# Performance work log

Hardware: AMD Instinct MI355X
Metric: run time of the kernel (lower is better)

## Reference

```python
import jax, jax.numpy as jnp
import numpy as np

KH = KW = 3
STRIDE, PAD, DIL = 1, 1, 1
HEADS, DG, CLIP, C = 12, 12, 2, 192
B, H, W = 4, 48, 48


def _linear_chw(x, w, b):
    # x: (n, d, c, h, w); Linear over channel dim (module rearranges to channels-last)
    return jnp.einsum('ndchw,oc->ndohw', x, w) + b[None, None, :, None, None]


def _deform_attn(q, kv, offset):
    # q: (b,1,C,H,W); kv: (b,clip,2C,H,W); offset: (b,clip,DG*K*2,H,W)
    b = q.shape[0]
    K = KH * KW
    HW = H * W
    dim = C // HEADS
    cg = 2 * C // DG  # channels per deformable group in kv (standard im2col split)
    ky = jnp.repeat(jnp.arange(KH), KW).astype(jnp.float32)  # (K,)
    kx = jnp.tile(jnp.arange(KW), KH).astype(jnp.float32)
    off = offset.reshape(b, CLIP, DG, K, 2, H, W)  # per-group [y,x] pairs per tap
    base_y = jnp.arange(H, dtype=jnp.float32)[None, :, None] * STRIDE - PAD + ky[:, None, None] * DIL  # (K,H,1)
    base_x = jnp.arange(W, dtype=jnp.float32)[None, None, :] * STRIDE - PAD + kx[:, None, None] * DIL  # (K,1,W)
    py = base_y + off[:, :, :, :, 0]  # (b,clip,dg,K,H,W)
    px = base_x + off[:, :, :, :, 1]
    kv_g = kv.reshape(b, CLIP, DG, cg, HW)

    y0 = jnp.floor(py)
    x0 = jnp.floor(px)
    wy1 = py - y0
    wx1 = px - x0

    def corner(yi, xi, wgt):
        valid = (yi >= 0) & (yi <= H - 1) & (xi >= 0) & (xi <= W - 1)
        idx = (jnp.clip(yi, 0, H - 1) * W + jnp.clip(xi, 0, W - 1)).astype(jnp.int32)
        idx = jnp.broadcast_to(idx.reshape(b, CLIP, DG, K, 1, HW), (b, CLIP, DG, K, cg, HW))
        src = jnp.broadcast_to(kv_g[:, :, :, None], (b, CLIP, DG, K, cg, HW))
        vals = jnp.take_along_axis(src, idx, axis=-1)  # gather over source pixels
        w_eff = (wgt * valid.astype(wgt.dtype)).reshape(b, CLIP, DG, K, 1, HW)
        return vals * w_eff

    s = (corner(y0, x0, (1 - wy1) * (1 - wx1))
         + corner(y0, x0 + 1, (1 - wy1) * wx1)
         + corner(y0 + 1, x0, wy1 * (1 - wx1))
         + corner(y0 + 1, x0 + 1, wy1 * wx1))  # (b,clip,dg,K,cg,HW)
    # restore channel order: (dg, cg) -> 2C = [C of k, C of v]
    s = s.transpose(0, 1, 2, 4, 3, 5).reshape(b, CLIP, 2, HEADS, dim, K, HW)
    ks, vs = s[:, :, 0], s[:, :, 1]  # (b,clip,heads,dim,K,HW)
    qh = q.reshape(b, HEADS, dim, HW) * (dim ** -0.5)
    scores = jnp.einsum('bhdn,bchdkn->bnhck', qh, ks)  # (b,HW,heads,clip,K)
    attn = jax.nn.softmax(scores.reshape(b, HW, HEADS, CLIP * K), axis=-1).reshape(b, HW, HEADS, CLIP, K)
    out = jnp.einsum('bnhck,bchdkn->bhdn', attn, vs)
    return out.reshape(b, 1, C, H, W)


def setup_inputs() -> dict:
    key = jax.random.key(0)
    ks = jax.random.split(key, 16)
    sd = 0.02
    return {
        'q': jax.random.normal(ks[0], (B, 1, C, H, W), jnp.float32),
        'k': jax.random.normal(ks[1], (B, CLIP, C, H, W), jnp.float32),
        'v': jax.random.normal(ks[2], (B, CLIP, C, H, W), jnp.float32),
        'offset': jax.random.normal(ks[3], (B, CLIP, DG * KH * KW * 2, H, W), jnp.float32),
        'wq': jax.random.normal(ks[4], (C, C), jnp.float32) * sd,
        'bq': jnp.zeros((C,), jnp.float32),
        'wk': jax.random.normal(ks[5], (C, C), jnp.float32) * sd,
        'bk': jnp.zeros((C,), jnp.float32),
        'wv': jax.random.normal(ks[6], (C, C), jnp.float32) * sd,
        'bv': jnp.zeros((C,), jnp.float32),
        'w1': jax.random.normal(ks[7], (2 * C, C), jnp.float32) * sd,
        'b1': jnp.zeros((2 * C,), jnp.float32),
        'w2': jax.random.normal(ks[8], (C, 2 * C), jnp.float32) * sd,
        'b2': jnp.zeros((C,), jnp.float32),
    }


def reference(q, k, v, offset, wq, bq, wk, bk, wv, bv, w1, b1, w2, b2):
    qp = _linear_chw(q, wq, bq)
    kv = jnp.concatenate([_linear_chw(k, wk, bk), _linear_chw(v, wv, bv)], axis=2)
    o = _deform_attn(qp, kv, offset)
    h = jnp.einsum('ndchw,oc->ndohw', o, w1) + b1[None, None, :, None, None]
    h = jax.nn.gelu(h, approximate=False)
    m = jnp.einsum('ndchw,oc->ndohw', h, w2) + b2[None, None, :, None, None]
    return o + m
```

## Files before the change

kernel.cpp:

```cpp
#include <hip/hip_runtime.h>

#define HW 2304
#define WID 48

typedef __attribute__((ext_vector_type(8))) short bf16x8;
typedef __attribute__((ext_vector_type(4))) float f32x4;
typedef __attribute__((ext_vector_type(2))) _Float16 half2v;

__device__ __forceinline__ half2v pk_h2(float lo, float hi) {
  return __builtin_bit_cast(half2v, __builtin_amdgcn_cvt_pkrtz(lo, hi));
}

__device__ __forceinline__ unsigned pack_bf2(float lo, float hi) {
  unsigned a = __builtin_bit_cast(unsigned, lo);
  unsigned b = __builtin_bit_cast(unsigned, hi);
  a = (a + 0x7FFFu + ((a >> 16) & 1u)) >> 16;
  b = (b + 0x7FFFu + ((b >> 16) & 1u)) >> 16;
  return a | (b << 16);
}
__device__ __forceinline__ unsigned short bf16_of(float x) {
  unsigned u = __builtin_bit_cast(unsigned, x);
  u = (u + 0x7FFFu + ((u >> 16) & 1u)) >> 16;
  return (unsigned short)u;
}
__device__ __forceinline__ unsigned short f16_of(float x) {
  _Float16 h = (_Float16)x;
  return __builtin_bit_cast(unsigned short, h);
}
__device__ __forceinline__ float lo_bf(unsigned u) {
  return __builtin_bit_cast(float, u << 16);
}
__device__ __forceinline__ float hi_bf(unsigned u) {
  return __builtin_bit_cast(float, u & 0xFFFF0000u);
}

__global__ __launch_bounds__(256) void prep_w(
    const float* __restrict__ wq, const float* __restrict__ wk,
    const float* __restrict__ wv, const float* __restrict__ w1,
    const float* __restrict__ w2, unsigned* __restrict__ wf)
{
  int fid = blockIdx.x * 4 + (threadIdx.x >> 6);
  int l = threadIdx.x & 63;
  const float* src; int K; int base;
  if (fid < 72)       { src = wq; K = 192; base = 0; }
  else if (fid < 144) { src = wk; K = 192; base = 72; }
  else if (fid < 216) { src = wv; K = 192; base = 144; }
  else if (fid < 360) { src = w1; K = 192; base = 216; }
  else                { src = w2; K = 384; base = 360; }
  int local = fid - base;
  int KS = K / 32;
  int nf = local / KS, ks = local % KS;
  int row = nf * 16 + (l & 15);
  int c0 = ks * 32 + (l >> 4) * 8;
  const float* p = src + (size_t)row * K + c0;
  float4 v0 = *(const float4*)p;
  float4 v1 = *(const float4*)(p + 4);
  unsigned* dst = wf + ((size_t)fid * 64 + l) * 4;
  dst[0] = pack_bf2(v0.x, v0.y);
  dst[1] = pack_bf2(v0.z, v0.w);
  dst[2] = pack_bf2(v1.x, v1.y);
  dst[3] = pack_bf2(v1.z, v1.w);
}

__global__ __launch_bounds__(256) void proj_mfma(
    const float* __restrict__ q, const float* __restrict__ k, const float* __restrict__ v,
    const unsigned* __restrict__ wf,
    const float* __restrict__ bq, const float* __restrict__ bk, const float* __restrict__ bv,
    float* __restrict__ qp, unsigned short* __restrict__ kvh)
{
  __shared__ unsigned lds[64 * 100];
  int slab = blockIdx.y;
  const float* in; const unsigned* wfr; const float* bias;
  float* outf = nullptr; unsigned short* outh = nullptr;
  int mode;
  if (slab < 4) {
    in = q + (size_t)slab * 192 * HW; wfr = wf; bias = bq;
    outf = qp + (size_t)slab * HW * 192; mode = 0;
  } else if (slab < 12) {
    int c = slab - 4;
    in = k + (size_t)c * 192 * HW; wfr = wf + 72 * 256; bias = bk;
    outh = kvh + (size_t)c * HW * 384; mode = 1;
  } else {
    int c = slab - 12;
    in = v + (size_t)c * 192 * HW; wfr = wf + 144 * 256; bias = bv;
    outh = kvh + (size_t)c * HW * 384 + 192; mode = 2;
  }
  const int n0 = blockIdx.x * 64;
  const int t = threadIdx.x;
  const int w = t >> 6, l = t & 63;

  {
    int pix = t & 63;
    int cp0 = t >> 6;
    const float* s0 = in + n0 + pix;
#pragma unroll
    for (int i = 0; i < 24; ++i) {
      int cp = cp0 * 24 + i;
      float lo = s0[(size_t)(2 * cp) * HW];
      float hi = s0[(size_t)(2 * cp + 1) * HW];
      lds[pix * 100 + cp] = pack_bf2(lo, hi);
    }
  }

  bf16x8 wfrag[6][3];
#pragma unroll
  for (int ks = 0; ks < 6; ++ks)
#pragma unroll
    for (int nfi = 0; nfi < 3; ++nfi) {
      int nf = w * 3 + nfi;
      wfrag[ks][nfi] = ((const bf16x8*)wfr)[(nf * 6 + ks) * 64 + l];
    }

  __syncthreads();

  f32x4 acc[3][4];
#pragma unroll
  for (int a = 0; a < 3; ++a)
#pragma unroll
    for (int m = 0; m < 4; ++m) acc[a][m] = (f32x4){0.f, 0.f, 0.f, 0.f};

#pragma unroll
  for (int ks = 0; ks < 6; ++ks) {
    bf16x8 af[4];
#pragma unroll
    for (int mf = 0; mf < 4; ++mf)
      af[mf] = *(const bf16x8*)&lds[(mf * 16 + (l & 15)) * 100 + ks * 16 + (l >> 4) * 4];
#pragma unroll
    for (int nfi = 0; nfi < 3; ++nfi)
#pragma unroll
      for (int mf = 0; mf < 4; ++mf)
        acc[nfi][mf] = __builtin_amdgcn_mfma_f32_16x16x32_bf16(af[mf], wfrag[ks][nfi], acc[nfi][mf], 0, 0, 0);
  }

#pragma unroll
  for (int nfi = 0; nfi < 3; ++nfi) {
    int oc = (w * 3 + nfi) * 16 + (l & 15);
    float bs = bias[oc];
    if (mode == 0) {
#pragma unroll
      for (int mf = 0; mf < 4; ++mf) {
        int pixb = n0 + mf * 16 + (l >> 4) * 4;
#pragma unroll
        for (int j = 0; j < 4; ++j)
          outf[(size_t)(pixb + j) * 192 + oc] = acc[nfi][mf][j] + bs;
      }
    } else if (mode == 1) {
#pragma unroll
      for (int mf = 0; mf < 4; ++mf) {
        int pixb = n0 + mf * 16 + (l >> 4) * 4;
#pragma unroll
        for (int j = 0; j < 4; ++j)
          outh[(size_t)(pixb + j) * 384 + oc] = f16_of(acc[nfi][mf][j] + bs);
      }
    } else {
#pragma unroll
      for (int mf = 0; mf < 4; ++mf) {
        int pixb = n0 + mf * 16 + (l >> 4) * 4;
#pragma unroll
        for (int j = 0; j < 4; ++j)
          outh[(size_t)(pixb + j) * 384 + oc] = bf16_of(acc[nfi][mf][j] + bs);
      }
    }
  }
}

__global__ __launch_bounds__(256, 4) void attn_kernel(
    const float* __restrict__ qp, const unsigned short* __restrict__ kvh,
    const float* __restrict__ offs, float* __restrict__ o_ws)
{
  __shared__ uint4 rec[2][2][9][32];
  const int t = threadIdx.x;
  const int g = blockIdx.x & 7;
  const int pos = blockIdx.x >> 3;
  const int b = g >> 1;
  const int half = g & 1;
  const int pk = pos / 36;
  const int tile = pos % 36;
  const int n_base = half * 1152 + tile * 32;

#pragma unroll
  for (int i = 0; i < 5; ++i) {
    int rid = t + i * 256;
    if (rid < 1152) {
      int rpix = rid & 31;
      int rest = rid >> 5;
      int rtap = rest % 9;
      int rq = rest / 9;
      int rclip = rq & 1;
      int dgsel = rq >> 1;
      int rn = n_base + rpix;
      int rh = rn / WID, rw = rn % WID;
      int dg = pk + dgsel * 6;
      const float* ob = offs + ((size_t)(b * 2 + rclip) * 216 + (size_t)(dg * 9 + rtap) * 2) * HW + rn;
      float oy = ob[0];
      float ox = ob[HW];
      float py = (float)(rh - 1 + rtap / 3) + oy;
      float px = (float)(rw - 1 + rtap % 3) + ox;
      float y0f = floorf(py), x0f = floorf(px);
      int y0 = (int)y0f, x0 = (int)x0f;
      float wy1 = py - y0f, wx1 = px - x0f;
      float wy0 = 1.f - wy1, wx0 = 1.f - wx1;
      unsigned ip[2];
      float wv[4];
#pragma unroll
      for (int cy = 0; cy < 2; ++cy) {
        int yi = y0 + cy;
        float wyv = cy ? wy1 : wy0;
        int yc = yi < 0 ? 0 : (yi > 47 ? 47 : yi);
        bool vy = (unsigned)yi < 48u;
#pragma unroll
        for (int cx = 0; cx < 2; ++cx) {
          int xi = x0 + cx;
          float wxv = cx ? wx1 : wx0;
          int xc = xi < 0 ? 0 : (xi > 47 ? 47 : xi);
          bool vx = (unsigned)xi < 48u;
          float wgt = (vy && vx) ? wyv * wxv : 0.f;
          int ci = cy * 2 + cx;
          wv[ci] = wgt;
          ((unsigned short*)ip)[ci] = (unsigned short)(yc * WID + xc);
        }
      }
      uint4 rc;
      rc.x = ip[0];
      rc.y = ip[1];
      rc.z = __builtin_bit_cast(unsigned, pk_h2(wv[0], wv[1]));
      rc.w = __builtin_bit_cast(unsigned, pk_h2(wv[2], wv[3]));
      rec[dgsel][rclip][rtap][rpix] = rc;
    }
  }

  const int sub = t & 3;
  const int hi = (t >> 2) & 1;
  const int pix = t >> 3;
  const int n = n_base + pix;
  const int h = 2 * pk + hi;

  half2v qh0, qh1;
  {
    float4 vv = *(const float4*)(qp + ((size_t)b * HW + n) * 192 + h * 16 + sub * 4);
    qh0 = pk_h2(vv.x * 0.25f, vv.y * 0.25f);
    qh1 = pk_h2(vv.z * 0.25f, vv.w * 0.25f);
  }

  __syncthreads();

  float sc[18];

#pragma unroll
  for (int c = 0; c < 2; ++c) {
    const unsigned short* kb = kvh + ((size_t)(b * 2 + c)) * HW * 384 + h * 16 + sub * 4;
#pragma unroll
    for (int kk = 0; kk < 9; ++kk) {
      uint4 rc = rec[0][c][kk][pix];
      half2v w01 = __builtin_bit_cast(half2v, rc.z);
      half2v w23 = __builtin_bit_cast(half2v, rc.w);
      float s = 0.f;
#pragma unroll
      for (int ci = 0; ci < 4; ++ci) {
        unsigned pr = (ci < 2) ? rc.x : rc.y;
        unsigned idx = (ci & 1) ? (pr >> 16) : (pr & 0xFFFFu);
        _Float16 wh = (ci == 0) ? w01.x : (ci == 1) ? w01.y : (ci == 2) ? w23.x : w23.y;
        uint2 u = *(const uint2*)(kb + (size_t)idx * 384);
        float d = __builtin_amdgcn_fdot2(qh0, __builtin_bit_cast(half2v, u.x), 0.f, false);
        d = __builtin_amdgcn_fdot2(qh1, __builtin_bit_cast(half2v, u.y), d, false);
        s += (float)wh * d;
      }
      s += __shfl_xor(s, 1, 64);
      s += __shfl_xor(s, 2, 64);
      sc[c * 9 + kk] = s;
    }
  }

  {
    float m = -1e30f;
#pragma unroll
    for (int j = 0; j < 18; ++j) m = fmaxf(m, sc[j]);
    float sum = 0.f;
#pragma unroll
    for (int j = 0; j < 18; ++j) { float ev = __expf(sc[j] - m); sc[j] = ev; sum += ev; }
    float inv = 1.f / sum;
#pragma unroll
    for (int j = 0; j < 18; ++j) sc[j] *= inv;
  }

  float ax = 0.f, ay = 0.f, az = 0.f, aw = 0.f;
#pragma unroll
  for (int c = 0; c < 2; ++c) {
    const unsigned short* vb = kvh + ((size_t)(b * 2 + c)) * HW * 384 + 192 + h * 16 + sub * 4;
#pragma unroll
    for (int kk = 0; kk < 9; ++kk) {
      uint4 rc = rec[1][c][kk][pix];
      half2v w01 = __builtin_bit_cast(half2v, rc.z);
      half2v w23 = __builtin_bit_cast(half2v, rc.w);
      float at = sc[c * 9 + kk];
#pragma unroll
      for (int ci = 0; ci < 4; ++ci) {
        unsigned pr = (ci < 2) ? rc.x : rc.y;
        unsigned idx = (ci & 1) ? (pr >> 16) : (pr & 0xFFFFu);
        _Float16 wh = (ci == 0) ? w01.x : (ci == 1) ? w01.y : (ci == 2) ? w23.x : w23.y;
        uint2 u = *(const uint2*)(vb + (size_t)idx * 384);
        float cw = (float)wh * at;
        ax += cw * lo_bf(u.x); ay += cw * hi_bf(u.x);
        az += cw * lo_bf(u.y); aw += cw * hi_bf(u.y);
      }
    }
  }

  float4 r; r.x = ax; r.y = ay; r.z = az; r.w = aw;
  *(float4*)(o_ws + ((size_t)b * HW + n) * 192 + h * 16 + sub * 4) = r;
}

__global__ __launch_bounds__(256) void mlp_mfma(
    const float* __restrict__ o_ws, const unsigned* __restrict__ wf,
    const float* __restrict__ b1, const float* __restrict__ b2,
    float* __restrict__ out)
{
  __shared__ unsigned ldsO[16 * 100];
  __shared__ unsigned ldsH[16 * 196];
  const unsigned* w1f = wf + 216 * 256;
  const unsigned* w2f = wf + 360 * 256;
  const int blk = blockIdx.x;
  const int b = blk / 144;
  const int n0 = (blk % 144) * 16;
  const int t = threadIdx.x;
  const int w = t >> 6, l = t & 63;

  for (int i = t; i < 16 * 96; i += 256) {
    int pix = i / 96, cp = i % 96;
    const float2 s = *(const float2*)(o_ws + ((size_t)(b * HW) + n0 + pix) * 192 + 2 * cp);
    ldsO[pix * 100 + cp] = pack_bf2(s.x, s.y);
  }
  __syncthreads();

  f32x4 acc1[6];
#pragma unroll
  for (int a = 0; a < 6; ++a) acc1[a] = (f32x4){0.f, 0.f, 0.f, 0.f};
#pragma unroll
  for (int ks = 0; ks < 6; ++ks) {
    bf16x8 af = *(const bf16x8*)&ldsO[(l & 15) * 100 + ks * 16 + (l >> 4) * 4];
#pragma unroll
    for (int nfi = 0; nfi < 6; ++nfi) {
      int nf = w * 6 + nfi;
      bf16x8 bfr = ((const bf16x8*)w1f)[(nf * 6 + ks) * 64 + l];
      acc1[nfi] = __builtin_amdgcn_mfma_f32_16x16x32_bf16(af, bfr, acc1[nfi], 0, 0, 0);
    }
  }

  {
    unsigned short* ldsHu = (unsigned short*)ldsH;
#pragma unroll
    for (int nfi = 0; nfi < 6; ++nfi) {
      int hc = (w * 6 + nfi) * 16 + (l & 15);
      float bs = b1[hc];
#pragma unroll
      for (int j = 0; j < 4; ++j) {
        int pix = (l >> 4) * 4 + j;
        float x = acc1[nfi][j] + bs;
        float gl = 0.5f * x * (1.f + erff(x * 0.70710678118654752f));
        ldsHu[pix * 392 + hc] = bf16_of(gl);
      }
    }
  }
  __syncthreads();

  f32x4 acc2[3];
#pragma unroll
  for (int a = 0; a < 3; ++a) acc2[a] = (f32x4){0.f, 0.f, 0.f, 0.f};
#pragma unroll
  for (int ks = 0; ks < 12; ++ks) {
    bf16x8 af = *(const bf16x8*)&ldsH[(l & 15) * 196 + ks * 16 + (l >> 4) * 4];
#pragma unroll
    for (int nfi = 0; nfi < 3; ++nfi) {
      int nf = w * 3 + nfi;
      bf16x8 bfr = ((const bf16x8*)w2f)[(nf * 12 + ks) * 64 + l];
      acc2[nfi] = __builtin_amdgcn_mfma_f32_16x16x32_bf16(af, bfr, acc2[nfi], 0, 0, 0);
    }
  }

#pragma unroll
  for (int nfi = 0; nfi < 3; ++nfi) {
    int oc = (w * 3 + nfi) * 16 + (l & 15);
    float bs = b2[oc];
#pragma unroll
    for (int j = 0; j < 4; ++j) {
      int pix = (l >> 4) * 4 + j;
      float res = o_ws[((size_t)(b * HW) + n0 + pix) * 192 + oc];
      out[((size_t)b * 192 + oc) * HW + n0 + pix] = acc2[nfi][j] + bs + res;
    }
  }
}

extern "C" void kernel_launch(void* const* d_in, const int* in_sizes, int n_in,
                              void* d_out, int out_size, void* d_ws, size_t ws_size,
                              hipStream_t stream) {
  const float* q = (const float*)d_in[0];
  const float* k = (const float*)d_in[1];
  const float* v = (const float*)d_in[2];
  const float* offset = (const float*)d_in[3];
  const float* wq = (const float*)d_in[4];
  const float* bq = (const float*)d_in[5];
  const float* wk = (const float*)d_in[6];
  const float* bk = (const float*)d_in[7];
  const float* wv = (const float*)d_in[8];
  const float* bv = (const float*)d_in[9];
  const float* w1 = (const float*)d_in[10];
  const float* b1 = (const float*)d_in[11];
  const float* w2 = (const float*)d_in[12];
  const float* b2 = (const float*)d_in[13];
  float* out = (float*)d_out;

  float* qp_t = (float*)d_ws;
  float* o_ws = qp_t + (size_t)4 * HW * 192;
  unsigned short* kvh = (unsigned short*)(o_ws + (size_t)4 * HW * 192);
  unsigned* wfb = (unsigned*)(kvh + (size_t)8 * HW * 384);

  dim3 blk(256);
  prep_w<<<dim3(126), blk, 0, stream>>>(wq, wk, wv, w1, w2, wfb);
  proj_mfma<<<dim3(36, 20), blk, 0, stream>>>(q, k, v, wfb, bq, bk, bv, qp_t, kvh);
  attn_kernel<<<dim3(1728), blk, 0, stream>>>(qp_t, kvh, offset, o_ws);
  mlp_mfma<<<dim3(576), blk, 0, stream>>>(o_ws, wfb, b1, b2, out);
}
```

Before: 76.52 us.

## Halve attention pixel tile to 16 and store V projection in fp16

The attention kernel now processes 16 pixels per block with 128 threads and launches twice as many blocks, with launch bounds raised to 8 blocks per CU. This is meant to improve occupancy and load balance for the gather-heavy sampling. The V projection is now stored as fp16 instead of bf16, matching K, so the attention inner loop converts with native half-to-float instead of bit shifts. The fp16 V storage changes precision and range, and only the visible parts of the attention kernel are adjusted to the new 16-pixel tiling.

```diff
diff --git a/kernel.cpp b/kernel.cpp
--- a/kernel.cpp
+++ b/kernel.cpp
@@ -26,12 +26,6 @@
 __device__ __forceinline__ unsigned short f16_of(float x) {
   _Float16 h = (_Float16)x;
   return __builtin_bit_cast(unsigned short, h);
-}
-__device__ __forceinline__ float lo_bf(unsigned u) {
-  return __builtin_bit_cast(float, u << 16);
-}
-__device__ __forceinline__ float hi_bf(unsigned u) {
-  return __builtin_bit_cast(float, u & 0xFFFF0000u);
 }
 
 __global__ __launch_bounds__(256) void prep_w(
@@ -72,18 +66,17 @@
   int slab = blockIdx.y;
   const float* in; const unsigned* wfr; const float* bias;
   float* outf = nullptr; unsigned short* outh = nullptr;
-  int mode;
   if (slab < 4) {
     in = q + (size_t)slab * 192 * HW; wfr = wf; bias = bq;
-    outf = qp + (size_t)slab * HW * 192; mode = 0;
+    outf = qp + (size_t)slab * HW * 192;
   } else if (slab < 12) {
     int c = slab - 4;
     in = k + (size_t)c * 192 * HW; wfr = wf + 72 * 256; bias = bk;
-    outh = kvh + (size_t)c * HW * 384; mode = 1;
+    outh = kvh + (size_t)c * HW * 384;
   } else {
     int c = slab - 12;
     in = v + (size_t)c * 192 * HW; wfr = wf + 144 * 256; bias = bv;
-    outh = kvh + (size_t)c * HW * 384 + 192; mode = 2;
+    outh = kvh + (size_t)c * HW * 384 + 192;
   }
   const int n0 = blockIdx.x * 64;
   const int t = threadIdx.x;
@@ -136,7 +129,7 @@
   for (int nfi = 0; nfi < 3; ++nfi) {
     int oc = (w * 3 + nfi) * 16 + (l & 15);
     float bs = bias[oc];
-    if (mode == 0) {
+    if (outf) {
 #pragma unroll
       for (int mf = 0; mf < 4; ++mf) {
         int pixb = n0 + mf * 16 + (l >> 4) * 4;
@@ -144,7 +137,7 @@
         for (int j = 0; j < 4; ++j)
           outf[(size_t)(pixb + j) * 192 + oc] = acc[nfi][mf][j] + bs;
       }
-    } else if (mode == 1) {
+    } else {
 #pragma unroll
       for (int mf = 0; mf < 4; ++mf) {
         int pixb = n0 + mf * 16 + (l >> 4) * 4;
@@ -152,38 +145,30 @@
         for (int j = 0; j < 4; ++j)
           outh[(size_t)(pixb + j) * 384 + oc] = f16_of(acc[nfi][mf][j] + bs);
       }
-    } else {
-#pragma unroll
-      for (int mf = 0; mf < 4; ++mf) {
-        int pixb = n0 + mf * 16 + (l >> 4) * 4;
-#pragma unroll
-        for (int j = 0; j < 4; ++j)
-          outh[(size_t)(pixb + j) * 384 + oc] = bf16_of(acc[nfi][mf][j] + bs);
-      }
-    }
-  }
-}
-
-__global__ __launch_bounds__(256, 4) void attn_kernel(
+    }
+  }
+}
+
+__global__ __launch_bounds__(128, 8) void attn_kernel(
     const float* __restrict__ qp, const unsigned short* __restrict__ kvh,
     const float* __restrict__ offs, float* __restrict__ o_ws)
 {
-  __shared__ uint4 rec[2][2][9][32];
+  __shared__ uint4 rec[2][2][9][16];
   const int t = threadIdx.x;
   const int g = blockIdx.x & 7;
   const int pos = blockIdx.x >> 3;
   const int b = g >> 1;
   const int half = g & 1;
-  const int pk = pos / 36;
-  const int tile = pos % 36;
-  const int n_base = half * 1152 + tile * 32;
+  const int pk = pos / 72;
+  const int tile = pos % 72;
+  const int n_base = half * 1152 + tile * 16;
 
 #pragma unroll
   for (int i = 0; i < 5; ++i) {
-    int rid = t + i * 256;
-    if (rid < 1152) {
-      int rpix = rid & 31;
-      int rest = rid >> 5;
+    int rid = t + i * 128;
+    if (rid < 576) {
+      int rpix = rid & 15;
+      int rest = rid >> 4;
       int rtap = rest % 9;
       int rq = rest / 9;
       int rclip = rq & 1;
@@ -299,9 +284,11 @@
         unsigned idx = (ci & 1) ? (pr >> 16) : (pr & 0xFFFFu);
         _Float16 wh = (ci == 0) ? w01.x : (ci == 1) ? w01.y : (ci == 2) ? w23.x : w23.y;
         uint2 u = *(const uint2*)(vb + (size_t)idx * 384);
+        half2v v01 = __builtin_bit_cast(half2v, u.x);
+        half2v v23 = __builtin_bit_cast(half2v, u.y);
         float cw = (float)wh * at;
-        ax += cw * lo_bf(u.x); ay += cw * hi_bf(u.x);
-        az += cw * lo_bf(u.y); aw += cw * hi_bf(u.y);
+        ax += cw * (float)v01.x; ay += cw * (float)v01.y;
+        az += cw * (float)v23.x; aw += cw * (float)v23.y;
       }
     }
   }
@@ -414,9 +401,8 @@
   unsigned short* kvh = (unsigned short*)(o_ws + (size_t)4 * HW * 192);
   unsigned* wfb = (unsigned*)(kvh + (size_t)8 * HW * 384);
 
-  dim3 blk(256);
-  prep_w<<<dim3(126), blk, 0, stream>>>(wq, wk, wv, w1, w2, wfb);
-  proj_mfma<<<dim3(36, 20), blk, 0, stream>>>(q, k, v, wfb, bq, bk, bv, qp_t, kvh);
-  attn_kernel<<<dim3(1728), blk, 0, stream>>>(qp_t, kvh, offset, o_ws);
-  mlp_mfma<<<dim3(576), blk, 0, stream>>>(o_ws, wfb, b1, b2, out);
-}
+  prep_w<<<dim3(126), dim3(256), 0, stream>>>(wq, wk, wv, w1, w2, wfb);
+  proj_mfma<<<dim3(36, 20), dim3(256), 0, stream>>>(q, k, v, wfb, bq, bk, bv, qp_t, kvh);
+  attn_kernel<<<dim3(3456), dim3(128), 0, stream>>>(qp_t, kvh, offset, o_ws);
+  mlp_mfma<<<dim3(576), dim3(256), 0, stream>>>(o_ws, wfb, b1, b2, out);
+}
```

New measurement: 81.92 us. +7.1%, slower.
